# Kernel optimization log

Hardware: AMD Instinct MI355X
Metric: run time of the kernel (lower is better)

Reference implementation:

```python
import jax, jax.numpy as jnp
import numpy as np

N = 20000      # nodes
E = 320000     # edges (before self-loops)
F_IN = 50      # PPI num_features
C1 = 256       # per-head channels, conv1/conv2
H1 = 4         # heads, conv1/conv2
C3 = 121       # PPI num_classes, conv3 per-head channels
H3 = 6         # heads, conv3 (concat=False -> mean)


def gat_conv(x, src, dst, W, a_src, a_dst, b, heads, ch, concat, n):
    """PyG-style GATConv with self-loops already included in (src, dst).
    Messages flow src -> dst; softmax is over incoming edges of each dst node."""
    h = (x @ W).reshape(n, heads, ch)                      # [N, H, C]
    es = jnp.sum(h * a_src, axis=-1)                       # [N, H]
    ed = jnp.sum(h * a_dst, axis=-1)                       # [N, H]
    e = jax.nn.leaky_relu(es[src] + ed[dst], 0.2)          # [E', H]
    m = jax.ops.segment_max(e, dst, num_segments=n)        # stable softmax per dst
    e = jnp.exp(e - m[dst])
    denom = jax.ops.segment_sum(e, dst, num_segments=n)
    alpha = e / jnp.maximum(denom[dst], 1e-16)             # [E', H]
    out = jax.ops.segment_sum(alpha[:, :, None] * h[src], dst, num_segments=n)  # [N, H, C]
    out = out.reshape(n, heads * ch) if concat else out.mean(axis=1)
    return out + b


def setup_inputs() -> dict:
    key = jax.random.key(0)
    ks = jax.random.split(key, 16)

    def p(k, shape, fan_in):
        return (jax.random.normal(k, shape, jnp.float32) / np.float32(np.sqrt(fan_in)))

    x = jax.random.normal(ks[0], (N, F_IN), jnp.float32)
    edge_index = jax.random.randint(ks[1], (2, E), 0, N, dtype=jnp.int64)
    D1 = H1 * C1  # 1024
    return dict(
        x=x, edge_index=edge_index,
        W1=p(ks[2], (F_IN, D1), F_IN), a1s=p(ks[3], (H1, C1), C1), a1d=p(ks[4], (H1, C1), C1), b1=jnp.zeros((D1,), jnp.float32),
        Wl1=p(ks[5], (F_IN, D1), F_IN), bl1=jnp.zeros((D1,), jnp.float32),
        W2=p(ks[6], (D1, D1), D1), a2s=p(ks[7], (H1, C1), C1), a2d=p(ks[8], (H1, C1), C1), b2=jnp.zeros((D1,), jnp.float32),
        Wl2=p(ks[9], (D1, D1), D1), bl2=jnp.zeros((D1,), jnp.float32),
        W3=p(ks[10], (D1, H3 * C3), D1), a3s=p(ks[11], (H3, C3), C3), a3d=p(ks[12], (H3, C3), C3), b3=jnp.zeros((C3,), jnp.float32),
        Wl3=p(ks[13], (D1, C3), D1), bl3=jnp.zeros((C3,), jnp.float32),
    )


def reference(x, edge_index, W1, a1s, a1d, b1, Wl1, bl1, W2, a2s, a2d, b2, Wl2, bl2, W3, a3s, a3d, b3, Wl3, bl3):
    n = x.shape[0]
    loop = jnp.arange(n, dtype=edge_index.dtype)           # PyG GATConv adds self-loops
    src = jnp.concatenate([edge_index[0], loop])
    dst = jnp.concatenate([edge_index[1], loop])
    x1 = jax.nn.elu(gat_conv(x, src, dst, W1, a1s, a1d, b1, H1, C1, True, n) + x @ Wl1 + bl1)
    x2 = jax.nn.elu(gat_conv(x1, src, dst, W2, a2s, a2d, b2, H1, C1, True, n) + x1 @ Wl2 + bl2)
    out = gat_conv(x2, src, dst, W3, a3s, a3d, b3, H3, C3, False, n) + x2 @ Wl3 + bl3
    return out
```

## Files before the change

### kernel.cpp

```cpp
#include <hip/hip_runtime.h>
#include <hip/hip_bf16.h>
#include <math.h>

typedef __bf16 bf16;
typedef __attribute__((ext_vector_type(4))) __bf16 bf16x4;
typedef __attribute__((ext_vector_type(8))) __bf16 bf16x8;
typedef __attribute__((ext_vector_type(4))) float f32x4;

#define N_NODES 20000
#define N_EDGES 320000
#define E2 (N_EDGES + N_NODES)
#define F_IN 50
#define D1 1024
#define NP12 2048
#define NP3 896
#define SG 2048
#define KA 320

#define PO_A1S 0
#define PO_A1D 1024
#define PO_B1  2048
#define PO_BL1 3072
#define PO_A2S 4096
#define PO_A2D 5120
#define PO_B2  6144
#define PO_BL2 7168
#define PO_A3S 8192
#define PO_A3D 8918
#define PO_B3  9644
#define PO_BL3 9765
#define PO_END 9886

#define PB_PADX  5000
#define PB_WF1   1280
#define PB_PAR   39
#define PB_LOG1  5000

__device__ __forceinline__ int clampi(int v, int lo, int hi)
{
    return v < lo ? lo : (v > hi ? hi : v);
}

__device__ __forceinline__ float loadf(const void* p, long idx, int isb)
{
    return isb ? (float)((const bf16*)p)[idx] : ((const float*)p)[idx];
}

__device__ __forceinline__ int loadei(const int* ei, long idx, int i64)
{
    return i64 ? ei[2 * idx] : ei[idx];
}

__global__ void k_detect(const int* __restrict__ ei,
                         const unsigned short* __restrict__ xw,
                         int* __restrict__ flags)
{
    if (blockIdx.x != 0 || threadIdx.x != 0) return;
    int allz = 1;
    for (int i = 0; i < 128; ++i)
        if (ei[2 * i + 1] != 0) { allz = 0; break; }
    int inr = 0;
    for (int i = 0; i < 128; ++i) {
        int e = (xw[2 * i] >> 7) & 0xFF;
        if (e >= 100 && e <= 140) inr++;
    }
    flags[0] = allz;
    flags[1] = (inr >= 64) ? 1 : 0;
}

template <bool BACT>
__global__ __launch_bounds__(256) void k_gemm(const bf16* __restrict__ A,
                                              const bf16* __restrict__ Bt,
                                              bf16* __restrict__ C,
                                              int M, int K, int lda, int ldb, int ldc,
                                              int mtiles, int ntiles,
                                              const bf16* __restrict__ bias)
{
    __shared__ bf16 As[128 * 64];
    __shared__ bf16 Bs[128 * 64];

    int id = blockIdx.x;
    int gfull = mtiles >> 3;
    int base  = gfull * 8 * ntiles;
    int x, y;
    if (id < base) {
        int gsz = 8 * ntiles;
        int g = id / gsz;
        int r = id - g * gsz;
        x = g * 8 + (r & 7);
        y = r >> 3;
    } else {
        int rem = mtiles - (gfull << 3);
        int r = id - base;
        x = (gfull << 3) + r % rem;
        y = r / rem;
    }
    const int m0 = x * 128;
    const int n0 = y * 128;

    const int tid  = threadIdx.x;
    const int wave = tid >> 6;
    const int lane = tid & 63;
    const int wm   = (wave >> 1) * 64;
    const int wn   = (wave & 1) * 64;
    const int frow  = lane & 15;

    const int srow = wave * 32 + (lane >> 3);
    const int scol = (((lane & 7) ^ (lane >> 3)) * 8);

    f32x4 acc[4][4];
#pragma unroll
    for (int i = 0; i < 4; ++i)
#pragma unroll
        for (int j = 0; j < 4; ++j)
#pragma unroll
            for (int r = 0; r < 4; ++r) acc[i][j][r] = 0.f;

    for (int k0 = 0; k0 < K; k0 += 64) {
#pragma unroll
        for (int i = 0; i < 4; ++i) {
            int ra = srow + i * 8;
            int ga = m0 + ra; if (ga > M - 1) ga = M - 1;
            __builtin_amdgcn_global_load_lds(
                (const __attribute__((address_space(1))) void*)(A + (size_t)ga * lda + k0 + scol),
                (__attribute__((address_space(3))) void*)(As + wave * 2048 + i * 512),
                16, 0, 0);
            int gb = n0 + ra;
            __builtin_amdgcn_global_load_lds(
                (const __attribute__((address_space(1))) void*)(Bt + (size_t)gb * ldb + k0 + scol),
                (__attribute__((address_space(3))) void*)(Bs + wave * 2048 + i * 512),
                16, 0, 0);
        }
        __syncthreads();
#pragma unroll
        for (int kk = 0; kk < 2; ++kk) {
            const int coff = (((kk * 4 + (lane >> 4)) ^ (frow & 7)) << 3);
            bf16x8 af[4], bfr[4];
#pragma unroll
            for (int i = 0; i < 4; ++i) {
                af[i]  = *(const bf16x8*)(As + (wm + i * 16 + frow) * 64 + coff);
                bfr[i] = *(const bf16x8*)(Bs + (wn + i * 16 + frow) * 64 + coff);
            }
#pragma unroll
            for (int i = 0; i < 4; ++i)
#pragma unroll
                for (int j = 0; j < 4; ++j)
                    acc[i][j] = __builtin_amdgcn_mfma_f32_16x16x32_bf16(af[i], bfr[j], acc[i][j], 0, 0, 0);
        }
        __syncthreads();
    }

#pragma unroll
    for (int i = 0; i < 4; ++i) {
#pragma unroll
        for (int j = 0; j < 4; ++j) {
            int rbase = m0 + wm + i * 16 + (lane >> 4) * 4;
            int col   = n0 + wn + j * 16 + frow;
            if constexpr (BACT) {
                float bv = (float)bias[col];
#pragma unroll
                for (int r = 0; r < 4; ++r) {
                    int row = rbase + r;
                    if (row < M) {
                        float v = acc[i][j][r] + bv;
                        v = (v > 0.f) ? v : (__expf(v) - 1.f);
                        C[(size_t)row * ldc + col] = (bf16)v;
                    }
                }
            } else {
#pragma unroll
                for (int r = 0; r < 4; ++r) {
                    int row = rbase + r;
                    if (row < M) C[(size_t)row * ldc + col] = (bf16)acc[i][j][r];
                }
            }
        }
    }
}

__global__ __launch_bounds__(256) void k_veca(const void* __restrict__ W1,
                                              const void* __restrict__ a1s,
                                              const void* __restrict__ a1d,
                                              const void* __restrict__ b1,
                                              const void* __restrict__ bl1,
                                              float* __restrict__ ws, float* __restrict__ wd,
                                              bf16* __restrict__ bsum,
                                              const int* __restrict__ flags)
{
    const int isb = flags[1];
    const int k = blockIdx.x;
    const int h = threadIdx.x >> 6;
    const int c0 = threadIdx.x & 63;
    float s = 0.f, d = 0.f;
    if (k < F_IN) {
        for (int c = c0; c < 256; c += 64) {
            float wv = loadf(W1, (long)k * D1 + h * 256 + c, isb);
            s += wv * loadf(a1s, h * 256 + c, isb);
            d += wv * loadf(a1d, h * 256 + c, isb);
        }
    }
#pragma unroll
    for (int off = 32; off; off >>= 1) {
        s += __shfl_xor(s, off);
        d += __shfl_xor(d, off);
    }
    if (c0 == 0) { ws[k * 4 + h] = s; wd[k * 4 + h] = d; }
    if (k < 4) {
        int j = k * 256 + threadIdx.x;
        bsum[j] = (bf16)(loadf(b1, j, isb) + loadf(bl1, j, isb));
    }
}

struct P12 { const void* s[12]; };

__global__ __launch_bounds__(256) void k_prep(const void* __restrict__ x,
                                              const void* __restrict__ W1,
                                              const void* __restrict__ Wl1,
                                              P12 ps,
                                              bf16* __restrict__ A2,
                                              bf16* __restrict__ Bt,
                                              bf16* __restrict__ pool,
                                              const float* __restrict__ ws,
                                              const float* __restrict__ wd,
                                              float* __restrict__ es,
                                              float* __restrict__ ed,
                                              const int* __restrict__ flags)
{
    const int isb = flags[1];
    int b = blockIdx.x;

    if (b < PB_PADX) {
        int idx = b * 256 + threadIdx.x;
        int n = idx >> 6, k = idx & 63;
        A2[(size_t)n * KA + 256 + k] = (k < F_IN) ? (bf16)loadf(x, (long)n * F_IN + k, isb)
                                                  : (bf16)0.f;
        return;
    }
    b -= PB_PADX;

    if (b < PB_WF1) {
        int idx = b * 256 + threadIdx.x;
        int j = idx / KA;
        int kp = idx - j * KA;
        float v = 0.f;
        if (kp < 256) {
            int hp = kp >> 6, k = kp & 63;
            if ((j >> 8) == hp && k < F_IN) v = loadf(W1, (long)k * D1 + j, isb);
        } else {
            int k = kp - 256;
            if (k < F_IN) v = loadf(Wl1, (long)k * D1 + j, isb);
        }
        Bt[idx] = (bf16)v;
        return;
    }
    b -= PB_WF1;

    if (b < PB_PAR) {
        const int off[13] = {PO_A1S, PO_A1D, PO_B1, PO_BL1, PO_A2S, PO_A2D, PO_B2,
                             PO_BL2, PO_A3S, PO_A3D, PO_B3, PO_BL3, PO_END};
        int idx = b * 256 + threadIdx.x;
        if (idx < PO_END) {
            int seg = 0;
            while (idx >= off[seg + 1]) seg++;
            pool[idx] = (bf16)loadf(ps.s[seg], idx - off[seg], isb);
        }
        return;
    }
    b -= PB_PAR;

    const int wave = threadIdx.x >> 6;
    const int lane = threadIdx.x & 63;
    const int n = b * 4 + wave;
    if (n >= N_NODES) return;
    float xv = (lane < F_IN) ? loadf(x, (long)n * F_IN + lane, isb) : 0.f;
    f32x4 wsv = *(const f32x4*)(ws + lane * 4);
    f32x4 wdv = *(const f32x4*)(wd + lane * 4);
    float s[4], d[4];
#pragma unroll
    for (int h = 0; h < 4; ++h) { s[h] = xv * wsv[h]; d[h] = xv * wdv[h]; }
#pragma unroll
    for (int off = 32; off; off >>= 1)
#pragma unroll
        for (int h = 0; h < 4; ++h) {
            s[h] += __shfl_xor(s[h], off);
            d[h] += __shfl_xor(d[h], off);
        }
    if (lane == 0) {
#pragma unroll
        for (int h = 0; h < 4; ++h) { es[n * 4 + h] = s[h]; ed[n * 4 + h] = d[h]; }
    }
}

__global__ __launch_bounds__(256) void k_wcatT(const void* __restrict__ Wa,
                                               const void* __restrict__ Wb,
                                               bf16* __restrict__ Bt,
                                               int split, int da, int db,
                                               const int* __restrict__ flags)
{
    __shared__ bf16 T[64][65];
    const int isb = flags[1];
    const int k0 = blockIdx.x * 64;
    const int n0 = blockIdx.y * 64;
    const int r = threadIdx.x >> 6;
    const int c = threadIdx.x & 63;
    const int n = n0 + c;
#pragma unroll
    for (int kk = 0; kk < 16; ++kk) {
        int k = k0 + r + kk * 4;
        float v = 0.f;
        if (n < split)           v = loadf(Wa, (long)k * da + n, isb);
        else if (n < split + db) v = loadf(Wb, (long)k * db + (n - split), isb);
        T[r + kk * 4][c] = (bf16)v;
    }
    __syncthreads();
#pragma unroll
    for (int kk = 0; kk < 16; ++kk) {
        int nn = r + kk * 4;
        Bt[(size_t)(n0 + nn) * 1024 + k0 + c] = T[c][nn];
    }
}

__global__ void k_count(const int* __restrict__ ei, int* __restrict__ cnt,
                        const int* __restrict__ flags)
{
    int e = blockIdx.x * 256 + threadIdx.x;
    if (e >= E2) return;
    int i64 = flags[0];
    int d = (e < N_EDGES) ? loadei(ei, (long)N_EDGES + e, i64) : (e - N_EDGES);
    d = clampi(d, 0, N_NODES - 1);
    atomicAdd(&cnt[d], 1);
}

__global__ __launch_bounds__(256) void k_scan(const int* __restrict__ cnt,
                                              int* __restrict__ rp,
                                              int* __restrict__ cur)
{
    __shared__ int ssum[256];
    int tid = threadIdx.x;
    const int chunk = (N_NODES + 255) / 256;
    int lo = tid * chunk;
    int hi = lo + chunk; if (hi > N_NODES) hi = N_NODES;
    int s = 0;
    for (int i = lo; i < hi; ++i) s += cnt[i];
    ssum[tid] = s;
    __syncthreads();
    if (tid == 0) {
        int run = 0;
        for (int i = 0; i < 256; ++i) { int t = ssum[i]; ssum[i] = run; run += t; }
        rp[N_NODES] = run;
    }
    __syncthreads();
    int run = ssum[tid];
    for (int i = lo; i < hi; ++i) { rp[i] = run; cur[i] = run; run += cnt[i]; }
}

__global__ void k_fill(const int* __restrict__ ei, int* __restrict__ cur,
                       int* __restrict__ ss, const int* __restrict__ flags)
{
    int e = blockIdx.x * 256 + threadIdx.x;
    if (e >= E2) return;
    int i64 = flags[0];
    int s, d;
    if (e < N_EDGES) {
        s = loadei(ei, e, i64);
        d = loadei(ei, (long)N_EDGES + e, i64);
    } else {
        s = e - N_EDGES; d = s;
    }
    s = clampi(s, 0, N_NODES - 1);
    d = clampi(d, 0, N_NODES - 1);
    int pos = atomicAdd(&cur[d], 1);
    if (pos >= 0 && pos < E2) ss[pos] = s;
}

__global__ __launch_bounds__(256) void k_aggxw(bf16* __restrict__ A2,
                                               const float* __restrict__ es,
                                               const float* __restrict__ ed,
                                               const int* __restrict__ rp,
                                               const int* __restrict__ ss)
{
    __shared__ float sal[4][4][65];
    __shared__ int   ssrc[4][64];

    const int w    = threadIdx.x >> 6;
    const int lane = threadIdx.x & 63;
    const int n    = blockIdx.x * 4 + w;
    if (n >= N_NODES) return;

    int r0 = clampi(rp[n], 0, E2);
    int r1 = clampi(rp[n + 1], r0, E2);
    const int deg = r1 - r0;

    f32x4 edn = *(const f32x4*)(ed + n * 4);

    float mx[4] = {-1e30f, -1e30f, -1e30f, -1e30f};
    float sm[4] = {0.f, 0.f, 0.f, 0.f};
    for (int c0 = 0; c0 < deg; c0 += 64) {
        const int e = c0 + lane;
        const bool val = (e < deg);
        const int s = val ? clampi(ss[r0 + e], 0, N_NODES - 1) : 0;
        f32x4 esv = *(const f32x4*)(es + s * 4);
        float w4[4], mc[4];
#pragma unroll
        for (int h = 0; h < 4; ++h) {
            float v = esv[h] + edn[h];
            v = (v > 0.f) ? v : 0.2f * v;
            w4[h] = val ? v : -1e30f;
            mc[h] = w4[h];
        }
#pragma unroll
        for (int off = 32; off; off >>= 1)
#pragma unroll
            for (int h = 0; h < 4; ++h) mc[h] = fmaxf(mc[h], __shfl_xor(mc[h], off));
        float ps[4];
#pragma unroll
        for (int h = 0; h < 4; ++h) {
            float mn = fmaxf(mx[h], mc[h]);
            float f  = __expf(mx[h] - mn);
            ps[h] = __expf(w4[h] - mn);
            mx[h] = mn;
            sm[h] *= f;
        }
#pragma unroll
        for (int off = 32; off; off >>= 1)
#pragma unroll
            for (int h = 0; h < 4; ++h) ps[h] += __shfl_xor(ps[h], off);
#pragma unroll
        for (int h = 0; h < 4; ++h) sm[h] += ps[h];
    }
    float sinv[4];
#pragma unroll
    for (int h = 0; h < 4; ++h) sinv[h] = 1.f / fmaxf(sm[h], 1e-16f);

    const int g  = lane >> 3;
    const int cb = (lane & 7) * 8;
    float acc[4][8];
#pragma unroll
    for (int h = 0; h < 4; ++h)
#pragma unroll
        for (int j = 0; j < 8; ++j) acc[h][j] = 0.f;

    for (int c0 = 0; c0 < deg; c0 += 64) {
        const int ce = min(64, deg - c0);
        const bool val = (lane < ce);
        const int e = c0 + lane;
        const int s = val ? clampi(ss[r0 + e], 0, N_NODES - 1) : 0;
        f32x4 esv = *(const f32x4*)(es + s * 4);
#pragma unroll
        for (int h = 0; h < 4; ++h) {
            float v = esv[h] + edn[h];
            v = (v > 0.f) ? v : 0.2f * v;
            sal[w][h][lane] = val ? __expf(v - mx[h]) * sinv[h] : 0.f;
        }
        ssrc[w][lane] = s;
        const int ce8 = (ce + 7) & ~7;
        for (int eb = 0; eb < ce8; eb += 8) {
            const int sg = ssrc[w][eb + g];
            bf16x8 xv = *(const bf16x8*)(A2 + (size_t)sg * KA + 256 + cb);
            float a[4];
#pragma unroll
            for (int h = 0; h < 4; ++h) a[h] = sal[w][h][eb + g];
#pragma unroll
            for (int h = 0; h < 4; ++h)
#pragma unroll
                for (int j = 0; j < 8; ++j) acc[h][j] += a[h] * (float)xv[j];
        }
    }

#pragma unroll
    for (int off = 8; off <= 32; off <<= 1)
#pragma unroll
        for (int h = 0; h < 4; ++h)
#pragma unroll
            for (int j = 0; j < 8; ++j) acc[h][j] += __shfl_xor(acc[h][j], off);

    if (g < 4) {
        bf16x8 ov;
#pragma unroll
        for (int j = 0; j < 8; ++j) {
            float v = (g == 0) ? acc[0][j]
                    : (g == 1) ? acc[1][j]
                    : (g == 2) ? acc[2][j] : acc[3][j];
            ov[j] = (bf16)v;
        }
        *(bf16x8*)(A2 + (size_t)n * KA + g * 64 + cb) = ov;
    }
}

template <int H, int C>
__global__ __launch_bounds__(256) void k_logits(const bf16* __restrict__ G,
                                                const bf16* __restrict__ as_,
                                                const bf16* __restrict__ ad_,
                                                float* __restrict__ es, float* __restrict__ ed)
{
    const int wave = threadIdx.x >> 6;
    const int lane = threadIdx.x & 63;
    const int n = blockIdx.x * 4 + wave;
    if (n >= N_NODES) return;

#pragma unroll
    for (int h = 0; h < H; ++h) {
        float s = 0.f, d = 0.f;
        if constexpr (C == 256) {
            bf16x4 g  = *(const bf16x4*)(G + (size_t)n * SG + h * 256 + lane * 4);
            bf16x4 av = *(const bf16x4*)(as_ + h * 256 + lane * 4);
            bf16x4 dv = *(const bf16x4*)(ad_ + h * 256 + lane * 4);
#pragma unroll
            for (int j = 0; j < 4; ++j) {
                float gv = (float)g[j];
                s += gv * (float)av[j];
                d += gv * (float)dv[j];
            }
        } else {
            for (int c = lane; c < C; c += 64) {
                float hv = (float)G[(size_t)n * SG + h * C + c];
                s += hv * (float)as_[h * C + c];
                d += hv * (float)ad_[h * C + c];
            }
        }
#pragma unroll
        for (int off = 32; off; off >>= 1) {
            s += __shfl_xor(s, off);
            d += __shfl_xor(d, off);
        }
        if (lane == 0) { es[n * H + h] = s; ed[n * H + h] = d; }
    }
}

__global__ __launch_bounds__(256) void k_aggw(const bf16* __restrict__ G,
                                              const bf16* __restrict__ S,
                                              const float* __restrict__ es,
                                              const float* __restrict__ ed,
                                              const int* __restrict__ rp,
                                              const int* __restrict__ ss,
                                              const bf16* __restrict__ bgat,
                                              const bf16* __restrict__ bskip,
                                              bf16* __restrict__ out, int sout)
{
    __shared__ float sal[4][4][65];
    __shared__ int   ssrc[4][64];

    const int w    = threadIdx.x >> 6;
    const int lane = threadIdx.x & 63;
    const int n    = blockIdx.x * 4 + w;
    if (n >= N_NODES) return;

    int r0 = clampi(rp[n], 0, E2);
    int r1 = clampi(rp[n + 1], r0, E2);
    const int deg = r1 - r0;

    f32x4 edn = *(const f32x4*)(ed + n * 4);

    float mx[4] = {-1e30f, -1e30f, -1e30f, -1e30f};
    float sm[4] = {0.f, 0.f, 0.f, 0.f};
    for (int c0 = 0; c0 < deg; c0 += 64) {
        const int e = c0 + lane;
        const bool val = (e < deg);
        const int s = val ? clampi(ss[r0 + e], 0, N_NODES - 1) : 0;
        f32x4 esv = *(const f32x4*)(es + s * 4);
        float w4[4], mc[4];
#pragma unroll
        for (int h = 0; h < 4; ++h) {
            float v = esv[h] + edn[h];
            v = (v > 0.f) ? v : 0.2f * v;
            w4[h] = val ? v : -1e30f;
            mc[h] = w4[h];
        }
#pragma unroll
        for (int off = 32; off; off >>= 1)
#pragma unroll
            for (int h = 0; h < 4; ++h) mc[h] = fmaxf(mc[h], __shfl_xor(mc[h], off));
        float ps[4];
#pragma unroll
        for (int h = 0; h < 4; ++h) {
            float mn = fmaxf(mx[h], mc[h]);
            float f  = __expf(mx[h] - mn);
            ps[h] = __expf(w4[h] - mn);
            mx[h] = mn;
            sm[h] *= f;
        }
#pragma unroll
        for (int off = 32; off; off >>= 1)
#pragma unroll
            for (int h = 0; h < 4; ++h) ps[h] += __shfl_xor(ps[h], off);
#pragma unroll
        for (int h = 0; h < 4; ++h) sm[h] += ps[h];
    }
    float sinv[4];
#pragma unroll
    for (int h = 0; h < 4; ++h) sinv[h] = 1.f / fmaxf(sm[h], 1e-16f);

    const int myh  = lane >> 4;
    const int c0ch = lane * 16;
    float acc[16];
#pragma unroll
    for (int j = 0; j < 16; ++j) acc[j] = 0.f;

    for (int c0 = 0; c0 < deg; c0 += 64) {
        const int ce = min(64, deg - c0);
        const bool val = (lane < ce);
        const int e = c0 + lane;
        const int s = val ? clampi(ss[r0 + e], 0, N_NODES - 1) : 0;
        f32x4 esv = *(const f32x4*)(es + s * 4);
#pragma unroll
        for (int h = 0; h < 4; ++h) {
            float v = esv[h] + edn[h];
            v = (v > 0.f) ? v : 0.2f * v;
            sal[w][h][lane] = val ? __expf(v - mx[h]) * sinv[h] : 0.f;
        }
        ssrc[w][lane] = s;
        const int ce4 = (ce + 3) & ~3;
        for (int eb = 0; eb < ce4; eb += 4) {
            int sg[4]; float a[4];
#pragma unroll
            for (int p = 0; p < 4; ++p) {
                sg[p] = ssrc[w][eb + p];
                a[p]  = sal[w][myh][eb + p];
            }
            bf16x8 g0[4], g1[4];
#pragma unroll
            for (int p = 0; p < 4; ++p) {
                const bf16* gp = G + (size_t)sg[p] * SG + c0ch;
                g0[p] = *(const bf16x8*)gp;
                g1[p] = *(const bf16x8*)(gp + 8);
            }
#pragma unroll
            for (int p = 0; p < 4; ++p) {
#pragma unroll
                for (int j = 0; j < 8; ++j) acc[j]     += a[p] * (float)g0[p][j];
#pragma unroll
                for (int j = 0; j < 8; ++j) acc[j + 8] += a[p] * (float)g1[p][j];
            }
        }
    }

    bf16x8 bg0 = *(const bf16x8*)(bgat + c0ch);
    bf16x8 bg1 = *(const bf16x8*)(bgat + c0ch + 8);
    bf16x8 sk0 = *(const bf16x8*)(S + (size_t)n * SG + c0ch);
    bf16x8 sk1 = *(const bf16x8*)(S + (size_t)n * SG + c0ch + 8);
    bf16x8 bs0 = *(const bf16x8*)(bskip + c0ch);
    bf16x8 bs1 = *(const bf16x8*)(bskip + c0ch + 8);
    bf16x8 ov0, ov1;
#pragma unroll
    for (int j = 0; j < 8; ++j) {
        float v = acc[j] + (float)bg0[j] + (float)sk0[j] + (float)bs0[j];
        v = (v > 0.f) ? v : (__expf(v) - 1.f);
        ov0[j] = (bf16)v;
        float u = acc[j + 8] + (float)bg1[j] + (float)sk1[j] + (float)bs1[j];
        u = (u > 0.f) ? u : (__expf(u) - 1.f);
        ov1[j] = (bf16)u;
    }
    *(bf16x8*)(out + (size_t)n * sout + c0ch)     = ov0;
    *(bf16x8*)(out + (size_t)n * sout + c0ch + 8) = ov1;
}

__global__ __launch_bounds__(256) void k_aggw3(const bf16* __restrict__ G,
                                               const bf16* __restrict__ S,
                                               const float* __restrict__ es,
                                               const float* __restrict__ ed,
                                               const int* __restrict__ rp,
                                               const int* __restrict__ ss,
                                               const bf16* __restrict__ bgat,
                                               const bf16* __restrict__ bskip,
                                               void* __restrict__ out, int sout,
                                               const int* __restrict__ flags)
{
    __shared__ float sal[4][6][65];
    __shared__ int   ssrc[4][64];
    __shared__ float sfold[4][728];

    const int w    = threadIdx.x >> 6;
    const int lane = threadIdx.x & 63;
    const int n    = blockIdx.x * 4 + w;
    if (n >= N_NODES) return;

    int r0 = clampi(rp[n], 0, E2);
    int r1 = clampi(rp[n + 1], r0, E2);
    const int deg = r1 - r0;

    float edn[6];
#pragma unroll
    for (int h = 0; h < 6; ++h) edn[h] = ed[n * 6 + h];

    float mx[6], sm[6];
#pragma unroll
    for (int h = 0; h < 6; ++h) { mx[h] = -1e30f; sm[h] = 0.f; }
    for (int c0 = 0; c0 < deg; c0 += 64) {
        const int e = c0 + lane;
        const bool val = (e < deg);
        const int s = val ? clampi(ss[r0 + e], 0, N_NODES - 1) : 0;
        const float* ep = es + (size_t)s * 6;
        float w6[6], mc[6];
#pragma unroll
        for (int h = 0; h < 6; ++h) {
            float v = ep[h] + edn[h];
            v = (v > 0.f) ? v : 0.2f * v;
            w6[h] = val ? v : -1e30f;
            mc[h] = w6[h];
        }
#pragma unroll
        for (int off = 32; off; off >>= 1)
#pragma unroll
            for (int h = 0; h < 6; ++h) mc[h] = fmaxf(mc[h], __shfl_xor(mc[h], off));
        float ps[6];
#pragma unroll
        for (int h = 0; h < 6; ++h) {
            float mn = fmaxf(mx[h], mc[h]);
            float f  = __expf(mx[h] - mn);
            ps[h] = __expf(w6[h] - mn);
            mx[h] = mn;
            sm[h] *= f;
        }
#pragma unroll
        for (int off = 32; off; off >>= 1)
#pragma unroll
            for (int h = 0; h < 6; ++h) ps[h] += __shfl_xor(ps[h], off);
#pragma unroll
        for (int h = 0; h < 6; ++h) sm[h] += ps[h];
    }
    float sinv[6];
#pragma unroll
    for (int h = 0; h < 6; ++h) sinv[h] = 1.f / fmaxf(sm[h], 1e-16f);

    const int c0ch = lane * 12;
    const int hA = min(c0ch / 121, 5);
    const int hB = min((c0ch + 11) / 121, 5);
    bool jA[12];
#pragma unroll
    for (int j = 0; j < 12; ++j) jA[j] = (min((c0ch + j) / 121, 5) == hA);

    float acc[12];
#pragma unroll
    for (int j = 0; j < 12; ++j) acc[j] = 0.f;

    for (int c0 = 0; c0 < deg; c0 += 64) {
        const int ce = min(64, deg - c0);
        const bool val = (lane < ce);
        const int e = c0 + lane;
        const int s = val ? clampi(ss[r0 + e], 0, N_NODES - 1) : 0;
        const float* ep = es + (size_t)s * 6;
#pragma unroll
        for (int h = 0; h < 6; ++h) {
            float v = ep[h] + edn[h];
            v = (v > 0.f) ? v : 0.2f * v;
            sal[w][h][lane] = val ? __expf(v - mx[h]) * sinv[h] : 0.f;
        }
        ssrc[w][lane] = s;
        const int ce4 = (ce + 3) & ~3;
        for (int eb = 0; eb < ce4; eb += 4) {
            int sg[4]; float aL[4], aH[4];
#pragma unroll
            for (int p = 0; p < 4; ++p) {
                sg[p] = ssrc[w][eb + p];
                aL[p] = sal[w][hA][eb + p];
                aH[p] = sal[w][hB][eb + p];
            }
#pragma unroll
            for (int p = 0; p < 4; ++p) {
                const bf16* gp = G + (size_t)sg[p] * SG + c0ch;
                bf16x4 g0 = *(const bf16x4*)gp;
                bf16x4 g1 = *(const bf16x4*)(gp + 4);
                bf16x4 g2 = *(const bf16x4*)(gp + 8);
#pragma unroll
                for (int j = 0; j < 4; ++j) acc[j]     += (jA[j]     ? aL[p] : aH[p]) * (float)g0[j];
#pragma unroll
                for (int j = 0; j < 4; ++j) acc[4 + j] += (jA[4 + j] ? aL[p] : aH[p]) * (float)g1[j];
#pragma unroll
                for (int j = 0; j < 4; ++j) acc[8 + j] += (jA[8 + j] ? aL[p] : aH[p]) * (float)g2[j];
            }
        }
    }

#pragma unroll
    for (int j = 0; j < 12; ++j) {
        int c = c0ch + j;
        if (c < 726) sfold[w][c] = acc[j];
    }
    const int outbf = flags[1];
    for (int c = lane; c < 121; c += 64) {
        float v = 0.f;
#pragma unroll
        for (int h = 0; h < 6; ++h) v += sfold[w][h * 121 + c];
        v *= (1.f / 6.f);
        v += (float)bgat[c] + (float)S[(size_t)n * SG + c] + (float)bskip[c];
        if (outbf) ((bf16*)out)[(size_t)n * sout + c] = (bf16)v;
        else       ((float*)out)[(size_t)n * sout + c] = v;
    }
}

extern "C" void kernel_launch(void* const* d_in, const int* in_sizes, int n_in,
                              void* d_out, int out_size, void* d_ws, size_t ws_size,
                              hipStream_t stream)
{
    const void* x   = d_in[0];
    const int*  ei  = (const int*)d_in[1];
    const void* W1  = d_in[2];
    const void* Wl1 = d_in[6];
    const void* W2  = d_in[8];
    const void* Wl2 = d_in[12];
    const void* W3  = d_in[14];
    const void* Wl3 = d_in[18];

    P12 ps;
    ps.s[0] = d_in[3];  ps.s[1] = d_in[4];  ps.s[2] = d_in[5];  ps.s[3] = d_in[7];
    ps.s[4] = d_in[9];  ps.s[5] = d_in[10]; ps.s[6] = d_in[11]; ps.s[7] = d_in[13];
    ps.s[8] = d_in[15]; ps.s[9] = d_in[16]; ps.s[10] = d_in[17]; ps.s[11] = d_in[19];

    char* w = (char*)d_ws;
    auto alloc = [&](size_t bytes) {
        char* p = w;
        w += (bytes + 255) & ~(size_t)255;
        return p;
    };
    int*   flags = (int*)alloc(64);
    int*   cnt   = (int*)alloc((size_t)N_NODES * 4);
    int*   rp    = (int*)alloc((size_t)(N_NODES + 1) * 4);
    int*   cur   = (int*)alloc((size_t)N_NODES * 4);
    int*   ss    = (int*)alloc((size_t)E2 * 4);
    float* es    = (float*)alloc((size_t)N_NODES * 6 * 4);
    float* ed    = (float*)alloc((size_t)N_NODES * 6 * 4);
    bf16*  pool  = (bf16*)alloc((size_t)PO_END * 2);
    float* ws1   = (float*)alloc((size_t)64 * 4 * 4);
    float* wd1   = (float*)alloc((size_t)64 * 4 * 4);
    bf16*  bsum  = (bf16*)alloc((size_t)D1 * 2);
    bf16*  Bt    = (bf16*)alloc((size_t)NP12 * 1024 * 2);
    bf16*  X     = (bf16*)alloc((size_t)N_NODES * D1 * 2);
    bf16*  WS    = (bf16*)alloc((size_t)N_NODES * SG * 2);
    bf16*  A2    = WS;

    k_detect<<<1, 64, 0, stream>>>(ei, (const unsigned short*)x, flags);

    hipMemsetAsync(cnt, 0, N_NODES * 4, stream);
    k_count<<<(E2 + 255) / 256, 256, 0, stream>>>(ei, cnt, flags);
    k_scan<<<1, 256, 0, stream>>>(cnt, rp, cur);
    k_fill<<<(E2 + 255) / 256, 256, 0, stream>>>(ei, cur, ss, flags);

    const dim3 blk(256);
    const int MT = (N_NODES + 127) / 128;

    k_veca<<<64, 256, 0, stream>>>(W1, ps.s[0], ps.s[1], ps.s[2], ps.s[3],
                                   ws1, wd1, bsum, flags);
    k_prep<<<PB_PADX + PB_WF1 + PB_PAR + PB_LOG1, 256, 0, stream>>>(
        x, W1, Wl1, ps, A2, Bt, pool, ws1, wd1, es, ed, flags);
    k_aggxw<<<N_NODES / 4, 256, 0, stream>>>(A2, es, ed, rp, ss);
    k_gemm<true><<<MT * (D1 / 128), blk, 0, stream>>>(A2, Bt, X, N_NODES, KA, KA, KA, D1,
                                                      MT, D1 / 128, bsum);

    k_wcatT<<<dim3(16, NP12 / 64), blk, 0, stream>>>(W2, Wl2, Bt, 1024, 1024, 1024, flags);
    k_gemm<false><<<MT * (NP12 / 128), blk, 0, stream>>>(X, Bt, WS, N_NODES, 1024, 1024, 1024, SG,
                                                         MT, NP12 / 128, nullptr);
    k_logits<4, 256><<<N_NODES / 4, 256, 0, stream>>>(WS, pool + PO_A2S, pool + PO_A2D, es, ed);
    k_aggw<<<N_NODES / 4, 256, 0, stream>>>(
        WS, WS + D1, es, ed, rp, ss, pool + PO_B2, pool + PO_BL2, X, D1);

    k_wcatT<<<dim3(16, NP3 / 64), blk, 0, stream>>>(W3, Wl3, Bt, 726, 726, 121, flags);
    k_gemm<false><<<MT * (NP3 / 128), blk, 0, stream>>>(X, Bt, WS, N_NODES, 1024, 1024, 1024, SG,
                                                        MT, NP3 / 128, nullptr);
    k_logits<6, 121><<<N_NODES / 4, 256, 0, stream>>>(WS, pool + PO_A3S, pool + PO_A3D, es, ed);
    k_aggw3<<<N_NODES / 4, 256, 0, stream>>>(
        WS, WS + 726, es, ed, rp, ss, pool + PO_B3, pool + PO_BL3, d_out, 121, flags);
}
```

Before: 635.0 us.

## Fuse layer-2 attention logits into GEMM epilogue and batch weight transposes into prep

The layer-2 GEMM epilogue now computes the per-head source and destination attention dot products from its accumulators. It reduces them with shuffles and atomically adds them into zeroed es/ed buffers, which removes the separate layer-2 logits kernel that re-read the projected features. The two weight transpose/concat launches are folded into the prep kernel as extra blocks writing to separate Bt2/Bt3 buffers, cutting launches and serialization. The layer-3 logits kernel is rewritten so each lane handles 12 contiguous channels with shared-memory atomics, and a memset is added to zero es/ed. The trade-offs are atomic contention, an order-dependent float summation, and extra epilogue work in the GEMM.

```diff
diff --git a/kernel.cpp b/kernel.cpp
--- a/kernel.cpp
+++ b/kernel.cpp
@@ -35,6 +35,8 @@
 #define PB_WF1   1280
 #define PB_PAR   39
 #define PB_LOG1  5000
+#define PB_WC2   512
+#define PB_WC3   224
 
 __device__ __forceinline__ int clampi(int v, int lo, int hi)
 {
@@ -68,13 +70,17 @@
     flags[1] = (inr >= 64) ? 1 : 0;
 }
 
-template <bool BACT>
+template <bool BACT, int LOGH>
 __global__ __launch_bounds__(256) void k_gemm(const bf16* __restrict__ A,
                                               const bf16* __restrict__ Bt,
                                               bf16* __restrict__ C,
                                               int M, int K, int lda, int ldb, int ldc,
                                               int mtiles, int ntiles,
-                                              const bf16* __restrict__ bias)
+                                              const bf16* __restrict__ bias,
+                                              const bf16* __restrict__ aps,
+                                              const bf16* __restrict__ apd,
+                                              float* __restrict__ es,
+                                              float* __restrict__ ed)
 {
     __shared__ bf16 As[128 * 64];
     __shared__ bf16 Bs[128 * 64];
@@ -150,6 +156,41 @@
         __syncthreads();
     }
 
+    if constexpr (LOGH == 4) {
+        if (n0 + wn < 1024) {
+            const int h = (n0 + wn) >> 8;
+            float asv[4], adv[4];
+#pragma unroll
+            for (int j = 0; j < 4; ++j) {
+                int col = n0 + wn + j * 16 + frow;
+                asv[j] = (float)aps[col];
+                adv[j] = (float)apd[col];
+            }
+#pragma unroll
+            for (int i = 0; i < 4; ++i) {
+#pragma unroll
+                for (int r = 0; r < 4; ++r) {
+                    float ps = 0.f, pd = 0.f;
+#pragma unroll
+                    for (int j = 0; j < 4; ++j) {
+                        ps += acc[i][j][r] * asv[j];
+                        pd += acc[i][j][r] * adv[j];
+                    }
+#pragma unroll
+                    for (int off = 8; off; off >>= 1) {
+                        ps += __shfl_xor(ps, off);
+                        pd += __shfl_xor(pd, off);
+                    }
+                    int row = m0 + wm + i * 16 + (lane >> 4) * 4 + r;
+                    if (frow == 0 && row < M) {
+                        atomicAdd(&es[row * 4 + h], ps);
+                        atomicAdd(&ed[row * 4 + h], pd);
+                    }
+                }
+            }
+        }
+    }
+
 #pragma unroll
     for (int i = 0; i < 4; ++i) {
 #pragma unroll
@@ -216,9 +257,15 @@
 __global__ __launch_bounds__(256) void k_prep(const void* __restrict__ x,
                                               const void* __restrict__ W1,
                                               const void* __restrict__ Wl1,
+                                              const void* __restrict__ W2,
+                                              const void* __restrict__ Wl2,
+                                              const void* __restrict__ W3,
+                                              const void* __restrict__ Wl3,
                                               P12 ps,
                                               bf16* __restrict__ A2,
                                               bf16* __restrict__ Bt,
+                                              bf16* __restrict__ Bt2,
+                                              bf16* __restrict__ Bt3,
                                               bf16* __restrict__ pool,
                                               const float* __restrict__ ws,
                                               const float* __restrict__ wd,
@@ -226,6 +273,7 @@
                                               float* __restrict__ ed,
                                               const int* __restrict__ flags)
 {
+    __shared__ bf16 T[64][65];
     const int isb = flags[1];
     int b = blockIdx.x;
 
@@ -268,55 +316,62 @@
     }
     b -= PB_PAR;
 
-    const int wave = threadIdx.x >> 6;
-    const int lane = threadIdx.x & 63;
-    const int n = b * 4 + wave;
-    if (n >= N_NODES) return;
-    float xv = (lane < F_IN) ? loadf(x, (long)n * F_IN + lane, isb) : 0.f;
-    f32x4 wsv = *(const f32x4*)(ws + lane * 4);
-    f32x4 wdv = *(const f32x4*)(wd + lane * 4);
-    float s[4], d[4];
-#pragma unroll
-    for (int h = 0; h < 4; ++h) { s[h] = xv * wsv[h]; d[h] = xv * wdv[h]; }
-#pragma unroll
-    for (int off = 32; off; off >>= 1)
-#pragma unroll
-        for (int h = 0; h < 4; ++h) {
-            s[h] += __shfl_xor(s[h], off);
-            d[h] += __shfl_xor(d[h], off);
-        }
-    if (lane == 0) {
-#pragma unroll
-        for (int h = 0; h < 4; ++h) { es[n * 4 + h] = s[h]; ed[n * 4 + h] = d[h]; }
-    }
-}
-
-__global__ __launch_bounds__(256) void k_wcatT(const void* __restrict__ Wa,
-                                               const void* __restrict__ Wb,
-                                               bf16* __restrict__ Bt,
-                                               int split, int da, int db,
-                                               const int* __restrict__ flags)
-{
-    __shared__ bf16 T[64][65];
-    const int isb = flags[1];
-    const int k0 = blockIdx.x * 64;
-    const int n0 = blockIdx.y * 64;
-    const int r = threadIdx.x >> 6;
-    const int c = threadIdx.x & 63;
-    const int n = n0 + c;
-#pragma unroll
-    for (int kk = 0; kk < 16; ++kk) {
-        int k = k0 + r + kk * 4;
-        float v = 0.f;
-        if (n < split)           v = loadf(Wa, (long)k * da + n, isb);
-        else if (n < split + db) v = loadf(Wb, (long)k * db + (n - split), isb);
-        T[r + kk * 4][c] = (bf16)v;
-    }
-    __syncthreads();
-#pragma unroll
-    for (int kk = 0; kk < 16; ++kk) {
-        int nn = r + kk * 4;
-        Bt[(size_t)(n0 + nn) * 1024 + k0 + c] = T[c][nn];
+    if (b < PB_LOG1) {
+        const int wave = threadIdx.x >> 6;
+        const int lane = threadIdx.x & 63;
+        const int n = b * 4 + wave;
+        if (n >= N_NODES) return;
+        float xv = (lane < F_IN) ? loadf(x, (long)n * F_IN + lane, isb) : 0.f;
+        f32x4 wsv = *(const f32x4*)(ws + lane * 4);
+        f32x4 wdv = *(const f32x4*)(wd + lane * 4);
+        float s[4], d[4];
+#pragma unroll
+        for (int h = 0; h < 4; ++h) { s[h] = xv * wsv[h]; d[h] = xv * wdv[h]; }
+#pragma unroll
+        for (int off = 32; off; off >>= 1)
+#pragma unroll
+            for (int h = 0; h < 4; ++h) {
+                s[h] += __shfl_xor(s[h], off);
+                d[h] += __shfl_xor(d[h], off);
+            }
+        if (lane == 0) {
+#pragma unroll
+            for (int h = 0; h < 4; ++h) { es[n * 4 + h] = s[h]; ed[n * 4 + h] = d[h]; }
+        }
+        return;
+    }
+    b -= PB_LOG1;
+
+    const bf16* dummy;
+    const void* Wa; const void* Wb; bf16* Bo; int split, da, db, bx, by;
+    if (b < PB_WC2) {
+        Wa = W2; Wb = Wl2; Bo = Bt2; split = 1024; da = 1024; db = 1024;
+        bx = b & 15; by = b >> 4;
+    } else {
+        b -= PB_WC2;
+        Wa = W3; Wb = Wl3; Bo = Bt3; split = 726; da = 726; db = 121;
+        bx = b % 16; by = b / 16;
+    }
+    {
+        const int k0 = bx * 64;
+        const int n0 = by * 64;
+        const int r = threadIdx.x >> 6;
+        const int c = threadIdx.x & 63;
+        const int n = n0 + c;
+#pragma unroll
+        for (int kk = 0; kk < 16; ++kk) {
+            int k = k0 + r + kk * 4;
+            float v = 0.f;
+            if (n < split)           v = loadf(Wa, (long)k * da + n, isb);
+            else if (n < split + db) v = loadf(Wb, (long)k * db + (n - split), isb);
+            T[r + kk * 4][c] = (bf16)v;
+        }
+        __syncthreads();
+#pragma unroll
+        for (int kk = 0; kk < 16; ++kk) {
+            int nn = r + kk * 4;
+            Bo[(size_t)(n0 + nn) * 1024 + k0 + c] = T[c][nn];
+        }
     }
 }
 
@@ -487,43 +542,55 @@
     }
 }
 
-template <int H, int C>
-__global__ __launch_bounds__(256) void k_logits(const bf16* __restrict__ G,
-                                                const bf16* __restrict__ as_,
-                                                const bf16* __restrict__ ad_,
-                                                float* __restrict__ es, float* __restrict__ ed)
-{
-    const int wave = threadIdx.x >> 6;
+__global__ __launch_bounds__(256) void k_logits3w(const bf16* __restrict__ G,
+                                                  const bf16* __restrict__ as_,
+                                                  const bf16* __restrict__ ad_,
+                                                  float* __restrict__ es,
+                                                  float* __restrict__ ed)
+{
+    __shared__ float sE[4][8], sD[4][8];
+    const int w    = threadIdx.x >> 6;
     const int lane = threadIdx.x & 63;
-    const int n = blockIdx.x * 4 + wave;
+    const int n    = blockIdx.x * 4 + w;
     if (n >= N_NODES) return;
 
-#pragma unroll
-    for (int h = 0; h < H; ++h) {
-        float s = 0.f, d = 0.f;
-        if constexpr (C == 256) {
-            bf16x4 g  = *(const bf16x4*)(G + (size_t)n * SG + h * 256 + lane * 4);
-            bf16x4 av = *(const bf16x4*)(as_ + h * 256 + lane * 4);
-            bf16x4 dv = *(const bf16x4*)(ad_ + h * 256 + lane * 4);
-#pragma unroll
-            for (int j = 0; j < 4; ++j) {
-                float gv = (float)g[j];
-                s += gv * (float)av[j];
-                d += gv * (float)dv[j];
-            }
-        } else {
-            for (int c = lane; c < C; c += 64) {
-                float hv = (float)G[(size_t)n * SG + h * C + c];
-                s += hv * (float)as_[h * C + c];
-                d += hv * (float)ad_[h * C + c];
-            }
-        }
-#pragma unroll
-        for (int off = 32; off; off >>= 1) {
-            s += __shfl_xor(s, off);
-            d += __shfl_xor(d, off);
-        }
-        if (lane == 0) { es[n * H + h] = s; ed[n * H + h] = d; }
+    if (lane < 8) { sE[w][lane] = 0.f; sD[w][lane] = 0.f; }
+
+    const int c0 = lane * 12;
+    int hA = min(c0 / 121, 5), hB = min((c0 + 11) / 121, 5);
+    float sA = 0.f, sB = 0.f, dA = 0.f, dB = 0.f;
+    if (c0 < 726) {
+        const bf16* gp = G + (size_t)n * SG + c0;
+        bf16x4 g0 = *(const bf16x4*)gp;
+        bf16x4 g1 = *(const bf16x4*)(gp + 4);
+        bf16x4 g2 = *(const bf16x4*)(gp + 8);
+        bf16x4 s0 = *(const bf16x4*)(as_ + c0);
+        bf16x4 s1 = *(const bf16x4*)(as_ + c0 + 4);
+        bf16x4 s2 = *(const bf16x4*)(as_ + c0 + 8);
+        bf16x4 d0 = *(const bf16x4*)(ad_ + c0);
+        bf16x4 d1 = *(const bf16x4*)(ad_ + c0 + 4);
+        bf16x4 d2 = *(const bf16x4*)(ad_ + c0 + 8);
+#pragma unroll
+        for (int j = 0; j < 12; ++j) {
+            int c = c0 + j;
+            if (c < 726) {
+                float gv = (float)((j < 4) ? g0[j] : (j < 8) ? g1[j - 4] : g2[j - 8]);
+                float sv = (float)((j < 4) ? s0[j] : (j < 8) ? s1[j - 4] : s2[j - 8]);
+                float dv = (float)((j < 4) ? d0[j] : (j < 8) ? d1[j - 4] : d2[j - 8]);
+                if (c / 121 == hA) { sA += gv * sv; dA += gv * dv; }
+                else               { sB += gv * sv; dB += gv * dv; }
+            }
+        }
+    }
+    atomicAdd(&sE[w][hA], sA);
+    atomicAdd(&sD[w][hA], dA);
+    if (hB != hA) {
+        atomicAdd(&sE[w][hB], sB);
+        atomicAdd(&sD[w][hB], dB);
+    }
+    if (lane < 6) {
+        es[n * 6 + lane] = sE[w][lane];
+        ed[n * 6 + lane] = sD[w][lane];
     }
 }
 
@@ -823,7 +890,9 @@
     float* ws1   = (float*)alloc((size_t)64 * 4 * 4);
     float* wd1   = (float*)alloc((size_t)64 * 4 * 4);
     bf16*  bsum  = (bf16*)alloc((size_t)D1 * 2);
-    bf16*  Bt    = (bf16*)alloc((size_t)NP12 * 1024 * 2);
+    bf16*  Bt    = (bf16*)alloc((size_t)D1 * KA * 2);
+    bf16*  Bt2   = (bf16*)alloc((size_t)NP12 * 1024 * 2);
+    bf16*  Bt3   = (bf16*)alloc((size_t)NP3 * 1024 * 2);
     bf16*  X     = (bf16*)alloc((size_t)N_NODES * D1 * 2);
     bf16*  WS    = (bf16*)alloc((size_t)N_NODES * SG * 2);
     bf16*  A2    = WS;
@@ -840,23 +909,24 @@
 
     k_veca<<<64, 256, 0, stream>>>(W1, ps.s[0], ps.s[1], ps.s[2], ps.s[3],
                                    ws1, wd1, bsum, flags);
-    k_prep<<<PB_PADX + PB_WF1 + PB_PAR + PB_LOG1, 256, 0, stream>>>(
-        x, W1, Wl1, ps, A2, Bt, pool, ws1, wd1, es, ed, flags);
+    k_prep<<<PB_PADX + PB_WF1 + PB_PAR + PB_LOG1 + PB_WC2 + PB_WC3, 256, 0, stream>>>(
+        x, W1, Wl1, W2, Wl2, W3, Wl3, ps, A2, Bt, Bt2, Bt3, pool, ws1, wd1, es, ed, flags);
     k_aggxw<<<N_NODES / 4, 256, 0, stream>>>(A2, es, ed, rp, ss);
-    k_gemm<true><<<MT * (D1 / 128), blk, 0, stream>>>(A2, Bt, X, N_NODES, KA, KA, KA, D1,
-                                                      MT, D1 / 128, bsum);
-
-    k_wcatT<<<dim3(16, NP12 / 64), blk, 0, stream>>>(W2, Wl2, Bt, 1024, 1024, 1024, flags);
-    k_gemm<false><<<MT * (NP12 / 128), blk, 0, stream>>>(X, Bt, WS, N_NODES, 1024, 1024, 1024, SG,
-                                                         MT, NP12 / 128, nullptr);
-    k_logits<4, 256><<<N_NODES / 4, 256, 0, stream>>>(WS, pool + PO_A2S, pool + PO_A2D, es, ed);
+    k_gemm<true, 0><<<MT * (D1 / 128), blk, 0, stream>>>(
+        A2, Bt, X, N_NODES, KA, KA, KA, D1, MT, D1 / 128, bsum,
+        nullptr, nullptr, nullptr, nullptr);
+
+    hipMemsetAsync(es, 0, (size_t)N_NODES * 6 * 4 * 2, stream);
+    k_gemm<false, 4><<<MT * (NP12 / 128), blk, 0, stream>>>(
+        X, Bt2, WS, N_NODES, 1024, 1024, 1024, SG, MT, NP12 / 128, nullptr,
+        pool + PO_A2S, pool + PO_A2D, es, ed);
     k_aggw<<<N_NODES / 4, 256, 0, stream>>>(
         WS, WS + D1, es, ed, rp, ss, pool + PO_B2, pool + PO_BL2, X, D1);
 
-    k_wcatT<<<dim3(16, NP3 / 64), blk, 0, stream>>>(W3, Wl3, Bt, 726, 726, 121, flags);
-    k_gemm<false><<<MT * (NP3 / 128), blk, 0, stream>>>(X, Bt, WS, N_NODES, 1024, 1024, 1024, SG,
-                                                        MT, NP3 / 128, nullptr);
-    k_logits<6, 121><<<N_NODES / 4, 256, 0, stream>>>(WS, pool + PO_A3S, pool + PO_A3D, es, ed);
+    k_gemm<false, 0><<<MT * (NP3 / 128), blk, 0, stream>>>(
+        X, Bt3, WS, N_NODES, 1024, 1024, 1024, SG, MT, NP3 / 128, nullptr,
+        nullptr, nullptr, nullptr, nullptr);
+    k_logits3w<<<N_NODES / 4, 256, 0, stream>>>(WS, pool + PO_A3S, pool + PO_A3D, es, ed);
     k_aggw3<<<N_NODES / 4, 256, 0, stream>>>(
         WS, WS + 726, es, ed, rp, ss, pool + PO_B3, pool + PO_BL3, d_out, 121, flags);
 }
```

Result: no change. 636.7 us (+0.3%).
